# Kernel optimization log

Measured on AMD Instinct MI355X. Metric: run time of the kernel, lower is better.

The kernel has to match this reference:

```python
import jax, jax.numpy as jnp
import numpy as np

CHUNK = 128
KERNEL_EPS = 1e-4
ATTN_EPS = 1e-6


def _gaussian_orthogonal_random_matrix(nb_rows, nb_cols, seed=0):
    # scaling=0: rows of stacked orthogonal blocks, scaled by chi-distributed norms
    rng = np.random.default_rng(seed)
    blocks = []
    n_full = nb_rows // nb_cols
    for _ in range(n_full):
        qm, _ = np.linalg.qr(rng.standard_normal((nb_cols, nb_cols)))
        blocks.append(qm.T)
    rem = nb_rows - n_full * nb_cols
    if rem > 0:
        qm, _ = np.linalg.qr(rng.standard_normal((nb_cols, nb_cols)))
        blocks.append(qm.T[:rem])
    mat = np.concatenate(blocks, axis=0)
    multiplier = np.linalg.norm(rng.standard_normal((nb_rows, nb_cols)), axis=1)
    return (multiplier[:, None] * mat).astype(np.float32)


def softmax_kernel(data, proj, is_query):
    # data: [b,h,n,d], proj: [m,d]
    d = data.shape[-1]
    m = proj.shape[0]
    data_normalizer = d ** -0.25
    ratio = m ** -0.5
    data_dash = jnp.einsum('bhnd,md->bhnm', data * data_normalizer, proj)
    diag_data = (data ** 2).sum(-1, keepdims=True) * 0.5 * (data_normalizer ** 2)
    if is_query:
        stab = jnp.max(data_dash, axis=-1, keepdims=True)
    else:
        stab = jnp.max(data_dash)
    return ratio * (jnp.exp(data_dash - diag_data - stab) + KERNEL_EPS)


def chunked_causal_linear_attention(qf, kf, v):
    # qf,kf: [b,h,n,m]; v: [b,h,n,e]
    b, h, n, m = qf.shape
    e = v.shape[-1]
    nc = n // CHUNK
    to_chunks = lambda t: t.reshape(b, h, nc, CHUNK, -1).transpose(2, 0, 1, 3, 4)
    qc, kc, vc = to_chunks(qf), to_chunks(kf), to_chunks(v)  # [nc,b,h,c,*]

    def step(carry, xs):
        Z, S = carry  # Z: [b,h,m], S: [b,h,m,e]
        q, k, vv = xs
        k_cum = Z[:, :, None, :] + jnp.cumsum(k, axis=2)          # [b,h,c,m]
        D_inv = 1.0 / jnp.einsum('bhcm,bhcm->bhc', q, k_cum + ATTN_EPS)
        ctx = jnp.einsum('bhcm,bhce->bhcme', k, vv)               # [b,h,c,m,e]
        ctx_cum = S[:, :, None, :, :] + jnp.cumsum(ctx, axis=2)
        out = jnp.einsum('bhcme,bhcm,bhc->bhce', ctx_cum, q, D_inv)
        return (k_cum[:, :, -1, :], ctx_cum[:, :, -1, :, :]), out

    Z0 = jnp.zeros((b, h, m), qf.dtype)
    S0 = jnp.zeros((b, h, m, e), qf.dtype)
    (Z, S), outs = jax.lax.scan(jax.checkpoint(step), (Z0, S0), (qc, kc, vc))
    out = outs.transpose(1, 2, 0, 3, 4).reshape(b, h, n, e)
    return out, Z, S


def setup_inputs() -> dict:
    key = jax.random.key(0)
    kq, kk, kv = jax.random.split(key, 3)
    B, H, N, D, M = 2, 8, 4096, 64, 256
    q = jax.random.normal(kq, (B, H, N, D), dtype=jnp.float32)
    k = jax.random.normal(kk, (B, H, N, D), dtype=jnp.float32)
    v = jax.random.normal(kv, (B, H, N, D), dtype=jnp.float32)
    projection_matrix = jnp.asarray(_gaussian_orthogonal_random_matrix(M, D))
    return {"q": q, "k": k, "v": v, "projection_matrix": projection_matrix,
            "inferrring_states": 1}


def reference(q, k, v, projection_matrix, inferrring_states):
    qf = softmax_kernel(q, projection_matrix, is_query=True)
    kf = softmax_kernel(k, projection_matrix, is_query=False)
    out, Z, S = chunked_causal_linear_attention(qf, kf, v)
    return (out, Z, S)
```

## Files before the change

kernel.cpp:

```cpp
#include <hip/hip_runtime.h>

typedef unsigned short ushort_t;
typedef __attribute__((ext_vector_type(8))) short bf16x8;
typedef __attribute__((ext_vector_type(8))) _Float16 f16x8;
typedef __attribute__((ext_vector_type(16))) float f32x16;

#define NORMC 0.35355339059327373f
#define DIAGC 0.0625f
#define RATIO 0.0625f
#define KEPS  1e-4f
#define AEPS  1e-6f
#define KAPPA (RATIO*KEPS)

__device__ __forceinline__ unsigned short f2bf(float f){
  unsigned u = __float_as_uint(f);
  unsigned r = (u + 0x7FFFu + ((u >> 16) & 1u)) >> 16;
  return (unsigned short)r;
}
__device__ __forceinline__ float bf2f(unsigned short h){
  return __uint_as_float(((unsigned)h) << 16);
}
__device__ __forceinline__ unsigned enc_f(float f){
  unsigned u = __float_as_uint(f);
  return (u & 0x80000000u) ? ~u : (u | 0x80000000u);
}
__device__ __forceinline__ float dec_f(unsigned e){
  unsigned b = (e & 0x80000000u) ? (e ^ 0x80000000u) : ~e;
  return __uint_as_float(b);
}
__device__ __forceinline__ unsigned short h2u(_Float16 h){
  union { _Float16 h; unsigned short u; } c; c.h = h; return c.u;
}
__device__ __forceinline__ unsigned pk2h(float a, float b){
  return (unsigned)h2u((_Float16)a) | ((unsigned)h2u((_Float16)b) << 16);
}

__global__ void k_prep(const float* __restrict__ proj, ushort_t* __restrict__ pjh,
                       unsigned* __restrict__ kmax){
  int t = threadIdx.x;
  if (t == 0) *kmax = 0u;
  for (int d = 0; d < 64; ++d){
    float val = NORMC * proj[t*64 + d];
    pjh[t*64 + d] = h2u((_Float16)val);
  }
}

__launch_bounds__(512, 4)
__global__ void k_featQ(const float* __restrict__ q, const ushort_t* __restrict__ pjh,
                        ushort_t* __restrict__ qf)
{
  extern __shared__ char sm[];
  char* Bp = sm;
  char* Xh = sm + 32768;
  char* Xl = sm + 49152;
  float* dsm = (float*)(sm + 65536);
  float* rmx = (float*)(sm + 66048);

  int tid = threadIdx.x;
  int w   = tid >> 6;
  int wr  = w & 3;
  int wc  = w >> 2;
  int lane= tid & 63;
  int l31 = lane & 31;
  int half= lane >> 5;
  int tile = (int)blockIdx.x;
  int row0 = tile * 128;

  for (int i = tid; i < 2048; i += 512){
    int m = i >> 3, c8 = i & 7;
    int rgn = ((m>>5)*4 + (c8>>1))*2 + (c8&1);
    int slot = (m & 31) ^ ((rgn & 7) << 2);
    *(uint4*)(Bp + rgn*512 + slot*16) = *(const uint4*)(pjh + m*64 + c8*8);
  }
  #pragma unroll
  for (int it = 0; it < 4; ++it){
    int g = it*512 + tid;
    int row = g >> 4, c4 = g & 15;
    float4 xv = *(const float4*)(q + (size_t)(row0+row)*64 + c4*4);
    _Float16 h0=(_Float16)xv.x, h1=(_Float16)xv.y, h2=(_Float16)xv.z, h3=(_Float16)xv.w;
    float l0 = xv.x-(float)h0, l1 = xv.y-(float)h1, l2 = xv.z-(float)h2, l3 = xv.w-(float)h3;
    int rgn = ((row>>5)*4 + (c4>>2))*2 + ((c4>>1)&1);
    int off = rgn*512 + (((row&31) ^ ((c4>>1)<<2)))*16 + (c4&1)*8;
    uint2 ph; ph.x = (unsigned)h2u(h0)|((unsigned)h2u(h1)<<16);
              ph.y = (unsigned)h2u(h2)|((unsigned)h2u(h3)<<16);
    uint2 pl; pl.x = pk2h(l0,l1); pl.y = pk2h(l2,l3);
    *(uint2*)(Xh + off) = ph;
    *(uint2*)(Xl + off) = pl;
    float ssq = xv.x*xv.x + xv.y*xv.y + xv.z*xv.z + xv.w*xv.w;
    ssq += __shfl_xor(ssq, 1); ssq += __shfl_xor(ssq, 2);
    ssq += __shfl_xor(ssq, 4); ssq += __shfl_xor(ssq, 8);
    if ((tid & 15) == 0) dsm[row] = ssq;
  }
  __syncthreads();

  f16x8 ah[4], al[4];
  #pragma unroll
  for (int ks = 0; ks < 4; ++ks){
    int rgn = (wr*4+ks)*2+half;
    int off = rgn*512 + ((l31 ^ ((2*ks+half)<<2)))*16;
    ah[ks] = *(const f16x8*)(Xh + off);
    al[ks] = *(const f16x8*)(Xl + off);
  }
  f32x16 acc[4];
  #pragma unroll
  for (int ct=0; ct<4; ++ct){
    #pragma unroll
    for (int r=0; r<16; ++r) acc[ct][r] = 0.f;
  }
  #pragma unroll
  for (int ks = 0; ks < 4; ++ks){
    #pragma unroll
    for (int ct=0; ct<4; ++ct){
      int ctg = wc*4 + ct;
      int rgn = (ctg*4+ks)*2+half;
      f16x8 bv = *(const f16x8*)(Bp + rgn*512 + ((l31 ^ ((2*ks+half)<<2)))*16);
      acc[ct] = __builtin_amdgcn_mfma_f32_32x32x16_f16(ah[ks], bv, acc[ct], 0, 0, 0);
      acc[ct] = __builtin_amdgcn_mfma_f32_32x32x16_f16(al[ks], bv, acc[ct], 0, 0, 0);
    }
  }
  {
    float rmax[16];
    #pragma unroll
    for (int r=0; r<16; ++r){
      float mx = acc[0][r];
      #pragma unroll
      for (int ct=1; ct<4; ++ct) mx = fmaxf(mx, acc[ct][r]);
      #pragma unroll
      for (int s=1; s<32; s<<=1) mx = fmaxf(mx, __shfl_xor(mx, s));
      rmax[r] = mx;
    }
    if (l31 == 0){
      #pragma unroll
      for (int r=0; r<16; ++r)
        rmx[wc*128 + 32*wr + (r&3) + 8*(r>>2) + 4*half] = rmax[r];
    }
  }
  __syncthreads();

  float dgv[16], stv[16];
  #pragma unroll
  for (int r=0; r<16; ++r){
    int lrow = 32*wr + (r&3) + 8*(r>>2) + 4*half;
    dgv[r] = DIAGC * dsm[lrow];
    stv[r] = fmaxf(rmx[lrow], rmx[128+lrow]);
  }

  char* ob = sm;
  #pragma unroll
  for (int r=0; r<16; ++r){
    int lrow = 32*wr + (r&3) + 8*(r>>2) + 4*half;
    #pragma unroll
    for (int ct=0; ct<4; ++ct){
      int col = wc*128 + ct*32 + l31;
      float e = __expf(acc[ct][r] - dgv[r] - stv[r]);
      *(ushort_t*)(ob + lrow*512 + ((col*2) ^ ((lrow&15)<<4))) = f2bf(RATIO*(e + KEPS));
    }
  }
  __syncthreads();
  ushort_t* dst = qf + (size_t)row0*256;
  for (int i = tid; i < 4096; i += 512){
    int row = i >> 5, s = i & 31;
    uint4 d = *(const uint4*)(ob + row*512 + ((s*16) ^ ((row&15)<<4)));
    *(uint4*)(dst + (size_t)row*256 + ((s ^ (row&15)))*8) = d;
  }
}

__launch_bounds__(512, 2)
__global__ void k_chunkF(const float* __restrict__ kk, const float* __restrict__ v,
                         const ushort_t* __restrict__ pjh,
                         ushort_t* __restrict__ kfp, float* __restrict__ Zl,
                         float* __restrict__ Sl, float* __restrict__ vsb,
                         unsigned* __restrict__ kmax, float* __restrict__ lmArr)
{
  extern __shared__ char sm[];
  char* Bp = sm;
  char* Xh = sm + 32768;
  char* Xl = sm + 49152;
  char* ob = sm;
  char* kT = sm + 65536;
  char* vT = sm + 131072;
  float* dsm  = (float*)(sm + 147456);
  float* wred = (float*)(sm + 147968);

  int tid = threadIdx.x;
  int w   = tid >> 6;
  int wr  = w & 3;
  int wc  = w >> 2;
  int lane= tid & 63;
  int l31 = lane & 31;
  int half= lane >> 5;
  int cb  = (int)blockIdx.x;
  int bh  = cb >> 5, j = cb & 31;
  int row0 = bh*4096 + j*128;

  for (int i = tid; i < 2048; i += 512){
    int m = i >> 3, c8 = i & 7;
    int rgn = ((m>>5)*4 + (c8>>1))*2 + (c8&1);
    int slot = (m & 31) ^ ((rgn & 7) << 2);
    *(uint4*)(Bp + rgn*512 + slot*16) = *(const uint4*)(pjh + m*64 + c8*8);
  }
  #pragma unroll
  for (int it = 0; it < 4; ++it){
    int g = it*512 + tid;
    int row = g >> 4, c4 = g & 15;
    float4 xv = *(const float4*)(kk + (size_t)(row0+row)*64 + c4*4);
    _Float16 h0=(_Float16)xv.x, h1=(_Float16)xv.y, h2=(_Float16)xv.z, h3=(_Float16)xv.w;
    float l0 = xv.x-(float)h0, l1 = xv.y-(float)h1, l2 = xv.z-(float)h2, l3 = xv.w-(float)h3;
    int rgn = ((row>>5)*4 + (c4>>2))*2 + ((c4>>1)&1);
    int off = rgn*512 + (((row&31) ^ ((c4>>1)<<2)))*16 + (c4&1)*8;
    uint2 ph; ph.x = (unsigned)h2u(h0)|((unsigned)h2u(h1)<<16);
              ph.y = (unsigned)h2u(h2)|((unsigned)h2u(h3)<<16);
    uint2 pl; pl.x = pk2h(l0,l1); pl.y = pk2h(l2,l3);
    *(uint2*)(Xh + off) = ph;
    *(uint2*)(Xl + off) = pl;
    float ssq = xv.x*xv.x + xv.y*xv.y + xv.z*xv.z + xv.w*xv.w;
    ssq += __shfl_xor(ssq, 1); ssq += __shfl_xor(ssq, 2);
    ssq += __shfl_xor(ssq, 4); ssq += __shfl_xor(ssq, 8);
    if ((tid & 15) == 0) dsm[row] = ssq;
  }
  {
    int e = tid & 63, c0 = tid >> 6;
    int swz = (e & 15) << 4;
    #pragma unroll
    for (int u=0; u<16; ++u){
      int c = c0 + u*8;
      *(ushort_t*)(vT + e*256 + ((c*2) ^ swz)) = f2bf(v[(size_t)(row0+c)*64 + e]);
    }
  }
  __syncthreads();

  f16x8 ah[4], al[4];
  #pragma unroll
  for (int ks = 0; ks < 4; ++ks){
    int rgn = (wr*4+ks)*2+half;
    int off = rgn*512 + ((l31 ^ ((2*ks+half)<<2)))*16;
    ah[ks] = *(const f16x8*)(Xh + off);
    al[ks] = *(const f16x8*)(Xl + off);
  }
  f32x16 acc[4];
  #pragma unroll
  for (int ct=0; ct<4; ++ct){
    #pragma unroll
    for (int r=0; r<16; ++r) acc[ct][r] = 0.f;
  }
  #pragma unroll
  for (int ks = 0; ks < 4; ++ks){
    #pragma unroll
    for (int ct=0; ct<4; ++ct){
      int ctg = wc*4 + ct;
      int rgn = (ctg*4+ks)*2+half;
      f16x8 bv = *(const f16x8*)(Bp + rgn*512 + ((l31 ^ ((2*ks+half)<<2)))*16);
      acc[ct] = __builtin_amdgcn_mfma_f32_32x32x16_f16(ah[ks], bv, acc[ct], 0, 0, 0);
      acc[ct] = __builtin_amdgcn_mfma_f32_32x32x16_f16(al[ks], bv, acc[ct], 0, 0, 0);
    }
  }
  {
    float wm = acc[0][0];
    #pragma unroll
    for (int ct=0; ct<4; ++ct){
      #pragma unroll
      for (int r=0; r<16; ++r) wm = fmaxf(wm, acc[ct][r]);
    }
    #pragma unroll
    for (int s=1; s<32; s<<=1) wm = fmaxf(wm, __shfl_xor(wm, s));
    wm = fmaxf(wm, __shfl_xor(wm, 32));
    if (lane == 0) wred[w] = wm;
  }
  __syncthreads();
  float lmb = wred[0];
  #pragma unroll
  for (int i=1;i<8;++i) lmb = fmaxf(lmb, wred[i]);
  if (tid == 0){
    lmArr[cb] = lmb;
    atomicMax(kmax, enc_f(lmb));
  }
  float dgv[16];
  #pragma unroll
  for (int r=0; r<16; ++r)
    dgv[r] = DIAGC * dsm[32*wr + (r&3) + 8*(r>>2) + 4*half];

  #pragma unroll
  for (int ct=0; ct<4; ++ct){
    int m = wc*128 + ct*32 + l31;
    int swm = (m & 15) << 4;
    #pragma unroll
    for (int g=0; g<4; ++g){
      unsigned pk0=0, pk1=0;
      #pragma unroll
      for (int rr=0; rr<4; ++rr){
        int r = g*4 + rr;
        int c = 32*wr + rr + 8*g + 4*half;
        float e = __expf(acc[ct][r] - dgv[r] - lmb);
        unsigned b = f2bf(e);
        if (rr < 2) pk0 |= b << (16*rr); else pk1 |= b << (16*(rr-2));
        *(ushort_t*)(ob + c*512 + ((m*2) ^ ((c&15)<<4))) = (ushort_t)b;
      }
      int c0 = 32*wr + 8*g + 4*half;
      *(uint2*)(kT + m*256 + ((c0*2) ^ swm)) = make_uint2(pk0, pk1);
    }
  }
  __syncthreads();

  f32x16 accS[2], accz, avs[2];
  #pragma unroll
  for (int et=0;et<2;++et){
    #pragma unroll
    for (int r=0;r<16;++r){ accS[et][r]=0.f; avs[et][r]=0.f; }
  }
  #pragma unroll
  for (int r=0;r<16;++r) accz[r]=0.f;
  bf16x8 onesB, onesA;
  #pragma unroll
  for (int i=0;i<8;++i){
    onesB[i] = (l31==0) ? (short)0x3F80 : (short)0;
    onesA[i] = (short)0x3F80;
  }
  int erow = (w&1)*32 + l31;
  int mc0  = ((w>>1)*2 + 0)*32 + l31;
  int mc1  = ((w>>1)*2 + 1)*32 + l31;
  int mrow = 32*w + l31;
  #pragma unroll
  for (int ks=0; ks<8; ++ks){
    int koff = ks*32 + half*16;
    bf16x8 afv = *(const bf16x8*)(vT + erow*256 + (koff ^ ((erow&15)<<4)));
    bf16x8 bk0 = *(const bf16x8*)(kT + mc0*256 + (koff ^ ((mc0&15)<<4)));
    bf16x8 bk1 = *(const bf16x8*)(kT + mc1*256 + (koff ^ ((mc1&15)<<4)));
    bf16x8 afk = *(const bf16x8*)(kT + mrow*256 + (koff ^ ((mrow&15)<<4)));
    accS[0] = __builtin_amdgcn_mfma_f32_32x32x16_bf16(afv, bk0, accS[0], 0, 0, 0);
    accS[1] = __builtin_amdgcn_mfma_f32_32x32x16_bf16(afv, bk1, accS[1], 0, 0, 0);
    accz    = __builtin_amdgcn_mfma_f32_32x32x16_bf16(afk, onesB, accz, 0, 0, 0);
    if (w == 0){
      bf16x8 bv1 = *(const bf16x8*)(vT + (32+l31)*256 + (koff ^ (((32+l31)&15)<<4)));
      avs[0] = __builtin_amdgcn_mfma_f32_32x32x16_bf16(onesA, afv, avs[0], 0, 0, 0);
      avs[1] = __builtin_amdgcn_mfma_f32_32x32x16_bf16(onesA, bv1, avs[1], 0, 0, 0);
    }
  }
  #pragma unroll
  for (int r=0; r<16; ++r){
    int e = (w&1)*32 + (r&3) + 8*(r>>2) + 4*half;
    Sl[(size_t)cb*16384 + (size_t)e*256 + ((w>>1)*2+0)*32 + l31] = accS[0][r];
    Sl[(size_t)cb*16384 + (size_t)e*256 + ((w>>1)*2+1)*32 + l31] = accS[1][r];
  }
  if (l31 == 0){
    #pragma unroll
    for (int r=0; r<16; ++r){
      int m = 32*w + (r&3) + 8*(r>>2) + 4*half;
      Zl[(size_t)cb*256 + m] = accz[r];
    }
  }
  if (w == 0 && half == 0){
    vsb[(size_t)cb*64 + l31]      = avs[0][0];
    vsb[(size_t)cb*64 + 32 + l31] = avs[1][0];
  }
  {
    ushort_t* dst = kfp + (size_t)row0*256;
    for (int i = tid; i < 4096; i += 512){
      int row = i >> 5, s = i & 31;
      uint4 d = *(const uint4*)(ob + row*512 + ((s*16) ^ ((row&15)<<4)));
      *(uint4*)(dst + (size_t)row*256 + ((s ^ (row&15)))*8) = d;
    }
  }
}

__launch_bounds__(256)
__global__ void k_scan(float* __restrict__ Zl, const float* __restrict__ Sl,
                       const float* __restrict__ vsb, const float* __restrict__ lmArr,
                       const unsigned* __restrict__ kmax,
                       ushort_t* __restrict__ S0b,
                       float* __restrict__ outZ, float* __restrict__ outSt){
  float gm = dec_f(*kmax);
  int t = threadIdx.x;
  int bh = blockIdx.x / 65;
  int s  = blockIdx.x % 65;
  if (s == 64){
    size_t base = (size_t)(bh*32)*256 + t;
    float rz = 0.f;
    #pragma unroll
    for (int j0=0;j0<32;j0+=8){
      float x[8];
      #pragma unroll
      for (int u=0;u<8;++u){
        int cbx = bh*32 + j0 + u;
        float a = RATIO * __expf(lmArr[cbx] - gm);
        x[u] = fmaf(a, Zl[base + (size_t)(j0+u)*256], KAPPA*128.f);
      }
      #pragma unroll
      for (int u=0;u<8;++u){ Zl[base + (size_t)(j0+u)*256] = rz; rz += x[u]; }
    }
    outZ[(size_t)bh*256 + t] = rz;
  } else {
    size_t base = (size_t)(bh*32)*16384 + (size_t)s*256 + t;
    float rs = 0.f;
    #pragma unroll
    for (int j0=0;j0<32;j0+=8){
      float x[8];
      #pragma unroll
      for (int u=0;u<8;++u){
        int cbx = bh*32 + j0 + u;
        float a = RATIO * __expf(lmArr[cbx] - gm);
        x[u] = fmaf(a, Sl[base + (size_t)(j0+u)*16384], KAPPA * vsb[(size_t)cbx*64 + s]);
      }
      #pragma unroll
      for (int u=0;u<8;++u){
        S0b[(size_t)(bh*32 + j0+u)*16384 + (size_t)s*256 + t] = f2bf(rs);
        rs += x[u];
      }
    }
    outSt[(size_t)bh*16384 + (size_t)s*256 + t] = rs;
  }
}

__launch_bounds__(256)
__global__ void k_tr(const float* __restrict__ outSt, float* __restrict__ outS){
  __shared__ float tl[64][65];
  int tid = threadIdx.x;
  int bh = blockIdx.x >> 2, mt = blockIdx.x & 3;
  int m0 = mt*64;
  for (int i = tid; i < 4096; i += 256){
    int e = i >> 6, m = i & 63;
    tl[e][m] = outSt[(size_t)bh*16384 + (size_t)e*256 + m0 + m];
  }
  __syncthreads();
  for (int i = tid; i < 4096; i += 256){
    int m = i >> 6, e = i & 63;
    outS[(size_t)bh*16384 + (size_t)(m0+m)*64 + e] = tl[e][m];
  }
}

__launch_bounds__(512, 2)
__global__ void k_out(const ushort_t* __restrict__ qf, const ushort_t* __restrict__ kfp,
                      const float* __restrict__ v, const ushort_t* __restrict__ S0b,
                      const float* __restrict__ Zp, const float* __restrict__ lmArr,
                      const unsigned* __restrict__ kmax, float* __restrict__ outO)
{
  extern __shared__ char sm[];
  char* Ab   = sm;
  char* qft  = sm + 32768;
  char* vTb  = sm + 32768;
  char* ktb  = sm + 49152;
  char* s0t  = sm + 65536;
  float* rsc = (float*)(sm + 73728);
  ushort_t* z0b = (ushort_t*)(sm + 74752);

  int tid = threadIdx.x;
  int w   = tid >> 6;
  int wr  = w & 3;
  int wc  = w >> 2;
  int lane= tid & 63;
  int l31 = lane & 31;
  int half= lane >> 5;
  int pb  = (int)blockIdx.x;
  int bh  = pb >> 5, j = pb & 31;
  int row0 = bh*4096 + j*128;
  size_t qbase = (size_t)row0*256;

  float gmv = dec_f(*kmax);
  float alpha = RATIO * __expf(lmArr[pb] - gmv);

  if (tid < 256) z0b[tid] = f2bf(Zp[(size_t)pb*256 + tid] + AEPS);

  int ve = tid & 63, vc0 = tid >> 6;
  float vld[16];
  #pragma unroll
  for (int u=0; u<16; ++u)
    vld[u] = v[(size_t)(row0 + vc0 + u*8)*64 + ve];

  int rr0 = (tid*2)   >> 3, c80 = (tid*2)   & 7;
  int rr1 = (tid*2+1) >> 3, c81 = (tid*2+1) & 7;
  int se  = tid >> 3,  sc8 = tid & 7;
  int dsw0 = (c80*16) ^ ((rr0&7)<<4);
  int dsw1 = (c81*16) ^ ((rr1&7)<<4);
  int dsws = (sc8*16) ^ ((se&7)<<4);

  uint4 pq0, pq1, pk0v, pk1v, ps0v;
  #define LOADT(m0_) do { \
    pq0  = *(const uint4*)(qf  + qbase + (size_t)rr0*256 + (m0_) + c80*8); \
    pq1  = *(const uint4*)(qf  + qbase + (size_t)rr1*256 + (m0_) + c81*8); \
    pk0v = *(const uint4*)(kfp + qbase + (size_t)rr0*256 + (m0_) + c80*8); \
    pk1v = *(const uint4*)(kfp + qbase + (size_t)rr1*256 + (m0_) + c81*8); \
    ps0v = *(const uint4*)(S0b + (size_t)pb*16384 + (size_t)se*256 + (m0_) + sc8*8); \
  } while(0)

  f32x16 accA[2], acc2, accQ;
  #pragma unroll
  for (int ct2=0;ct2<2;++ct2){
    #pragma unroll
    for (int r=0;r<16;++r) accA[ct2][r] = 0.f;
  }
  #pragma unroll
  for (int r=0;r<16;++r){ acc2[r] = 0.f; accQ[r] = 0.f; }

  int arow = 32*wr + l31;
  LOADT(0);

  #pragma unroll
  for (int mt=0; mt<4; ++mt){
    int m0 = mt*64;
    __syncthreads();
    *(uint4*)(qft + rr0*128 + dsw0) = pq0;
    *(uint4*)(qft + rr1*128 + dsw1) = pq1;
    *(uint4*)(ktb + rr0*128 + dsw0) = pk0v;
    *(uint4*)(ktb + rr1*128 + dsw1) = pk1v;
    *(uint4*)(s0t + se*128  + dsws) = ps0v;
    __syncthreads();
    if (mt < 3) LOADT((mt+1)*64);
    #pragma unroll
    for (int ks=0;ks<4;++ks){
      int ko = ks*32 + half*16;
      bf16x8 af = *(const bf16x8*)(qft + arow*128 + (ko ^ ((arow&7)<<4)));
      {
        int er = wc*32 + l31;
        bf16x8 bS = *(const bf16x8*)(s0t + er*128 + (ko ^ ((er&7)<<4)));
        acc2 = __builtin_amdgcn_mfma_f32_32x32x16_bf16(af, bS, acc2, 0, 0, 0);
      }
      {
        bf16x8 zb = {};
        if (l31 == 0) zb = *(const bf16x8*)((const char*)z0b + m0*2 + ko);
        if (l31 == 1){
          #pragma unroll
          for (int i2=0;i2<8;++i2) zb[i2] = (short)0x3F80;
        }
        accQ = __builtin_amdgcn_mfma_f32_32x32x16_bf16(af, zb, accQ, 0, 0, 0);
      }
      #pragma unroll
      for (int ct2=0;ct2<2;++ct2){
        int c = wc*2 + ct2;
        if (c <= wr){
          int br = c*32 + l31;
          bf16x8 bk = *(const bf16x8*)(ktb + br*128 + (ko ^ ((br&7)<<4)));
          accA[ct2] = __builtin_amdgcn_mfma_f32_32x32x16_bf16(af, bk, accA[ct2], 0, 0, 0);
        }
      }
    }
  }
  #undef LOADT

  float qzv[16], qfsv[16];
  #pragma unroll
  for (int r=0;r<16;++r){
    qzv[r]  = __shfl(accQ[r], half*32 + 0);
    qfsv[r] = __shfl(accQ[r], half*32 + 1);
  }

  {
    float p[16];
    #pragma unroll
    for (int r=0;r<16;++r) p[r]=0.f;
    #pragma unroll
    for (int ct2=0;ct2<2;++ct2){
      int c = wc*2 + ct2;
      if (c <= wr){
        #pragma unroll
        for (int r=0;r<16;++r){
          int grow = 32*wr + (r&3) + 8*(r>>2) + 4*half;
          int col  = c*32 + l31;
          float mval = (col <= grow) ? fmaf(alpha, accA[ct2][r], KAPPA*qfsv[r]) : 0.f;
          p[r] += mval;
          *(ushort_t*)(Ab + grow*256 + ((col*2) ^ ((grow&15)<<4))) = f2bf(mval);
        }
      }
    }
    #pragma unroll
    for (int s2=1;s2<32;s2<<=1){
      #pragma unroll
      for (int r=0;r<16;++r) p[r] += __shfl_xor(p[r], s2);
    }
    if (l31 == 0){
      #pragma unroll
      for (int r=0;r<16;++r)
        rsc[wc*128 + 32*wr + (r&3) + 8*(r>>2) + 4*half] = p[r];
    }
  }
  __syncthreads();

  {
    int swz = (ve & 15) << 4;
    #pragma unroll
    for (int u=0; u<16; ++u){
      int c = vc0 + u*8;
      *(ushort_t*)(vTb + ve*256 + ((c*2) ^ swz)) = f2bf(vld[u]);
    }
  }
  __syncthreads();

  #pragma unroll
  for (int ks=0; ks<8; ++ks){
    if (ks <= 2*wr + 1){
      bf16x8 af = *(const bf16x8*)(Ab + arow*256 + ((ks*32 + half*16) ^ ((arow&15)<<4)));
      int er = wc*32 + l31;
      bf16x8 bv = *(const bf16x8*)(vTb + er*256 + ((ks*32 + half*16) ^ ((er&15)<<4)));
      acc2 = __builtin_amdgcn_mfma_f32_32x32x16_bf16(af, bv, acc2, 0, 0, 0);
    }
  }

  #pragma unroll
  for (int r=0;r<16;++r){
    int grow = 32*wr + (r&3) + 8*(r>>2) + 4*half;
    float dv = 1.0f / (rsc[grow] + rsc[128+grow] + qzv[r]);
    outO[(size_t)(row0+grow)*64 + wc*32 + l31] = acc2[r] * dv;
  }
}

extern "C" void kernel_launch(void* const* d_in, const int* in_sizes, int n_in,
                              void* d_out, int out_size, void* d_ws, size_t ws_size,
                              hipStream_t stream){
  (void)in_sizes; (void)n_in; (void)out_size; (void)ws_size;
  const float* q    = (const float*)d_in[0];
  const float* k    = (const float*)d_in[1];
  const float* v    = (const float*)d_in[2];
  const float* proj = (const float*)d_in[3];

  char* ws = (char*)d_ws;
  unsigned* kmax = (unsigned*)ws;
  float*    lmA  = (float*)(ws + 256);
  ushort_t* pjh  = (ushort_t*)(ws + 4096);
  ushort_t* kfp  = (ushort_t*)(ws + 65792);
  float*    Zl   = (float*)(ws + 33620224);
  float*    Sl   = (float*)(ws + 34144512);
  ushort_t* S0b  = (ushort_t*)(ws + 67698944);
  float*    vsb  = (float*)(ws + 84476160);
  float*    oSt  = (float*)(ws + 84607232);
  ushort_t* qfb  = (ushort_t*)(ws + 88801536);

  float* outO = (float*)d_out;
  float* outZ = outO + (size_t)2*8*4096*64;
  float* outS = outZ + 2*8*256;

  hipFuncSetAttribute((const void*)k_featQ,  hipFuncAttributeMaxDynamicSharedMemorySize, 67072);
  hipFuncSetAttribute((const void*)k_chunkF, hipFuncAttributeMaxDynamicSharedMemorySize, 148480);
  hipFuncSetAttribute((const void*)k_out,    hipFuncAttributeMaxDynamicSharedMemorySize, 75264);

  k_prep  <<<1,     256, 0, stream>>>(proj, pjh, kmax);
  k_featQ <<<512,   512, 67072, stream>>>(q, pjh, qfb);
  k_chunkF<<<512,   512, 148480, stream>>>(k, v, pjh, kfp, Zl, Sl, vsb, kmax, lmA);
  k_scan  <<<16*65, 256, 0, stream>>>(Zl, Sl, vsb, lmA, kmax, S0b, outZ, oSt);
  k_tr    <<<64,    256, 0, stream>>>(oSt, outS);
  k_out   <<<512,   512, 75264, stream>>>(qfb, kfp, v, S0b, Zl, lmA, kmax, outO);
}
```

Baseline: 106.8 us.

## Split k_out Q·S0 and Q·K passes to cut register pressure

The single fused loop over the feature dimension, which held accA[2], acc2 and accQ live together, is split into two passes: first Q·S0 and Q·Z, then Q·K^T. The per-row normaliser values go through shared memory instead of registers. V is now loaded just before its transpose rather than held in 16 registers across the whole kernel. The launch-bounds hint asks for 4 blocks per SM instead of 2. The aim is higher occupancy, at the cost of reloading the Q tiles a second time, extra barriers, and a slightly larger shared-memory footprint that may itself cap residency.

```diff
diff --git a/kernel.cpp b/kernel.cpp
--- a/kernel.cpp
+++ b/kernel.cpp
@@ -427,7 +427,7 @@
   }
 }
 
-__launch_bounds__(512, 2)
+__launch_bounds__(512, 4)
 __global__ void k_out(const ushort_t* __restrict__ qf, const ushort_t* __restrict__ kfp,
                       const float* __restrict__ v, const ushort_t* __restrict__ S0b,
                       const float* __restrict__ Zp, const float* __restrict__ lmArr,
@@ -441,6 +441,8 @@
   char* s0t  = sm + 65536;
   float* rsc = (float*)(sm + 73728);
   ushort_t* z0b = (ushort_t*)(sm + 74752);
+  float* qzl = (float*)(sm + 75264);
+  float* qfl = (float*)(sm + 75776);
 
   int tid = threadIdx.x;
   int w   = tid >> 6;
@@ -459,102 +461,126 @@
 
   if (tid < 256) z0b[tid] = f2bf(Zp[(size_t)pb*256 + tid] + AEPS);
 
-  int ve = tid & 63, vc0 = tid >> 6;
-  float vld[16];
-  #pragma unroll
-  for (int u=0; u<16; ++u)
-    vld[u] = v[(size_t)(row0 + vc0 + u*8)*64 + ve];
-
   int rr0 = (tid*2)   >> 3, c80 = (tid*2)   & 7;
   int rr1 = (tid*2+1) >> 3, c81 = (tid*2+1) & 7;
   int se  = tid >> 3,  sc8 = tid & 7;
   int dsw0 = (c80*16) ^ ((rr0&7)<<4);
   int dsw1 = (c81*16) ^ ((rr1&7)<<4);
   int dsws = (sc8*16) ^ ((se&7)<<4);
-
-  uint4 pq0, pq1, pk0v, pk1v, ps0v;
-  #define LOADT(m0_) do { \
-    pq0  = *(const uint4*)(qf  + qbase + (size_t)rr0*256 + (m0_) + c80*8); \
-    pq1  = *(const uint4*)(qf  + qbase + (size_t)rr1*256 + (m0_) + c81*8); \
-    pk0v = *(const uint4*)(kfp + qbase + (size_t)rr0*256 + (m0_) + c80*8); \
-    pk1v = *(const uint4*)(kfp + qbase + (size_t)rr1*256 + (m0_) + c81*8); \
-    ps0v = *(const uint4*)(S0b + (size_t)pb*16384 + (size_t)se*256 + (m0_) + sc8*8); \
-  } while(0)
-
-  f32x16 accA[2], acc2, accQ;
+  int arow = 32*wr + l31;
+
+  f32x16 acc2, accQ;
+  #pragma unroll
+  for (int r=0;r<16;++r){ acc2[r] = 0.f; accQ[r] = 0.f; }
+  {
+    uint4 pq0, pq1, ps0;
+    pq0 = *(const uint4*)(qf  + qbase + (size_t)rr0*256 + c80*8);
+    pq1 = *(const uint4*)(qf  + qbase + (size_t)rr1*256 + c81*8);
+    ps0 = *(const uint4*)(S0b + (size_t)pb*16384 + (size_t)se*256 + sc8*8);
+    #pragma unroll
+    for (int mt=0; mt<4; ++mt){
+      int m0 = mt*64;
+      __syncthreads();
+      *(uint4*)(qft + rr0*128 + dsw0) = pq0;
+      *(uint4*)(qft + rr1*128 + dsw1) = pq1;
+      *(uint4*)(s0t + se*128  + dsws) = ps0;
+      __syncthreads();
+      if (mt < 3){
+        int mn = (mt+1)*64;
+        pq0 = *(const uint4*)(qf  + qbase + (size_t)rr0*256 + mn + c80*8);
+        pq1 = *(const uint4*)(qf  + qbase + (size_t)rr1*256 + mn + c81*8);
+        ps0 = *(const uint4*)(S0b + (size_t)pb*16384 + (size_t)se*256 + mn + sc8*8);
+      }
+      #pragma unroll
+      for (int ks=0;ks<4;++ks){
+        int ko = ks*32 + half*16;
+        bf16x8 af = *(const bf16x8*)(qft + arow*128 + (ko ^ ((arow&7)<<4)));
+        {
+          int er = wc*32 + l31;
+          bf16x8 bS = *(const bf16x8*)(s0t + er*128 + (ko ^ ((er&7)<<4)));
+          acc2 = __builtin_amdgcn_mfma_f32_32x32x16_bf16(af, bS, acc2, 0, 0, 0);
+        }
+        {
+          bf16x8 zb = {};
+          if (l31 == 0) zb = *(const bf16x8*)((const char*)z0b + m0*2 + ko);
+          if (l31 == 1){
+            #pragma unroll
+            for (int i2=0;i2<8;++i2) zb[i2] = (short)0x3F80;
+          }
+          accQ = __builtin_amdgcn_mfma_f32_32x32x16_bf16(af, zb, accQ, 0, 0, 0);
+        }
+      }
+    }
+  }
+  #pragma unroll
+  for (int r=0;r<16;++r){
+    float qz  = __shfl(accQ[r], half*32 + 0);
+    float qfs = __shfl(accQ[r], half*32 + 1);
+    if (wc == 0 && l31 == 0){
+      int grow = 32*wr + (r&3) + 8*(r>>2) + 4*half;
+      qzl[grow] = qz;
+      qfl[grow] = qfs;
+    }
+  }
+
+  f32x16 accA[2];
   #pragma unroll
   for (int ct2=0;ct2<2;++ct2){
     #pragma unroll
     for (int r=0;r<16;++r) accA[ct2][r] = 0.f;
   }
-  #pragma unroll
-  for (int r=0;r<16;++r){ acc2[r] = 0.f; accQ[r] = 0.f; }
-
-  int arow = 32*wr + l31;
-  LOADT(0);
-
-  #pragma unroll
-  for (int mt=0; mt<4; ++mt){
-    int m0 = mt*64;
-    __syncthreads();
-    *(uint4*)(qft + rr0*128 + dsw0) = pq0;
-    *(uint4*)(qft + rr1*128 + dsw1) = pq1;
-    *(uint4*)(ktb + rr0*128 + dsw0) = pk0v;
-    *(uint4*)(ktb + rr1*128 + dsw1) = pk1v;
-    *(uint4*)(s0t + se*128  + dsws) = ps0v;
-    __syncthreads();
-    if (mt < 3) LOADT((mt+1)*64);
-    #pragma unroll
-    for (int ks=0;ks<4;++ks){
-      int ko = ks*32 + half*16;
-      bf16x8 af = *(const bf16x8*)(qft + arow*128 + (ko ^ ((arow&7)<<4)));
-      {
-        int er = wc*32 + l31;
-        bf16x8 bS = *(const bf16x8*)(s0t + er*128 + (ko ^ ((er&7)<<4)));
-        acc2 = __builtin_amdgcn_mfma_f32_32x32x16_bf16(af, bS, acc2, 0, 0, 0);
-      }
-      {
-        bf16x8 zb = {};
-        if (l31 == 0) zb = *(const bf16x8*)((const char*)z0b + m0*2 + ko);
-        if (l31 == 1){
-          #pragma unroll
-          for (int i2=0;i2<8;++i2) zb[i2] = (short)0x3F80;
+  {
+    uint4 pq0, pq1, pk0v, pk1v;
+    pq0  = *(const uint4*)(qf  + qbase + (size_t)rr0*256 + c80*8);
+    pq1  = *(const uint4*)(qf  + qbase + (size_t)rr1*256 + c81*8);
+    pk0v = *(const uint4*)(kfp + qbase + (size_t)rr0*256 + c80*8);
+    pk1v = *(const uint4*)(kfp + qbase + (size_t)rr1*256 + c81*8);
+    #pragma unroll
+    for (int mt=0; mt<4; ++mt){
+      __syncthreads();
+      *(uint4*)(qft + rr0*128 + dsw0) = pq0;
+      *(uint4*)(qft + rr1*128 + dsw1) = pq1;
+      *(uint4*)(ktb + rr0*128 + dsw0) = pk0v;
+      *(uint4*)(ktb + rr1*128 + dsw1) = pk1v;
+      __syncthreads();
+      if (mt < 3){
+        int mn = (mt+1)*64;
+        pq0  = *(const uint4*)(qf  + qbase + (size_t)rr0*256 + mn + c80*8);
+        pq1  = *(const uint4*)(qf  + qbase + (size_t)rr1*256 + mn + c81*8);
+        pk0v = *(const uint4*)(kfp + qbase + (size_t)rr0*256 + mn + c80*8);
+        pk1v = *(const uint4*)(kfp + qbase + (size_t)rr1*256 + mn + c81*8);
+      }
+      #pragma unroll
+      for (int ks=0;ks<4;++ks){
+        int ko = ks*32 + half*16;
+        bf16x8 af = *(const bf16x8*)(qft + arow*128 + (ko ^ ((arow&7)<<4)));
+        #pragma unroll
+        for (int ct2=0;ct2<2;++ct2){
+          int c = wc*2 + ct2;
+          if (c <= wr){
+            int br = c*32 + l31;
+            bf16x8 bk = *(const bf16x8*)(ktb + br*128 + (ko ^ ((br&7)<<4)));
+            accA[ct2] = __builtin_amdgcn_mfma_f32_32x32x16_bf16(af, bk, accA[ct2], 0, 0, 0);
+          }
         }
-        accQ = __builtin_amdgcn_mfma_f32_32x32x16_bf16(af, zb, accQ, 0, 0, 0);
-      }
+      }
+    }
+  }
+
+  {
+    float p[16];
+    #pragma unroll
+    for (int r=0;r<16;++r) p[r]=0.f;
+    #pragma unroll
+    for (int r=0;r<16;++r){
+      int grow = 32*wr + (r&3) + 8*(r>>2) + 4*half;
+      float qfs = qfl[grow];
       #pragma unroll
       for (int ct2=0;ct2<2;++ct2){
         int c = wc*2 + ct2;
         if (c <= wr){
-          int br = c*32 + l31;
-          bf16x8 bk = *(const bf16x8*)(ktb + br*128 + (ko ^ ((br&7)<<4)));
-          accA[ct2] = __builtin_amdgcn_mfma_f32_32x32x16_bf16(af, bk, accA[ct2], 0, 0, 0);
-        }
-      }
-    }
-  }
-  #undef LOADT
-
-  float qzv[16], qfsv[16];
-  #pragma unroll
-  for (int r=0;r<16;++r){
-    qzv[r]  = __shfl(accQ[r], half*32 + 0);
-    qfsv[r] = __shfl(accQ[r], half*32 + 1);
-  }
-
-  {
-    float p[16];
-    #pragma unroll
-    for (int r=0;r<16;++r) p[r]=0.f;
-    #pragma unroll
-    for (int ct2=0;ct2<2;++ct2){
-      int c = wc*2 + ct2;
-      if (c <= wr){
-        #pragma unroll
-        for (int r=0;r<16;++r){
-          int grow = 32*wr + (r&3) + 8*(r>>2) + 4*half;
-          int col  = c*32 + l31;
-          float mval = (col <= grow) ? fmaf(alpha, accA[ct2][r], KAPPA*qfsv[r]) : 0.f;
+          int col = c*32 + l31;
+          float mval = (col <= grow) ? fmaf(alpha, accA[ct2][r], KAPPA*qfs) : 0.f;
           p[r] += mval;
           *(ushort_t*)(Ab + grow*256 + ((col*2) ^ ((grow&15)<<4))) = f2bf(mval);
         }
@@ -574,11 +600,13 @@
   __syncthreads();
 
   {
+    int ve = tid & 63, vc0 = tid >> 6;
     int swz = (ve & 15) << 4;
     #pragma unroll
     for (int u=0; u<16; ++u){
       int c = vc0 + u*8;
-      *(ushort_t*)(vTb + ve*256 + ((c*2) ^ swz)) = f2bf(vld[u]);
+      float vv = v[(size_t)(row0 + c)*64 + ve];
+      *(ushort_t*)(vTb + ve*256 + ((c*2) ^ swz)) = f2bf(vv);
     }
   }
   __syncthreads();
@@ -596,7 +624,7 @@
   #pragma unroll
   for (int r=0;r<16;++r){
     int grow = 32*wr + (r&3) + 8*(r>>2) + 4*half;
-    float dv = 1.0f / (rsc[grow] + rsc[128+grow] + qzv[r]);
+    float dv = 1.0f / (rsc[grow] + rsc[128+grow] + qzl[grow]);
     outO[(size_t)(row0+grow)*64 + wc*32 + l31] = acc2[r] * dv;
   }
 }
@@ -628,12 +656,12 @@
 
   hipFuncSetAttribute((const void*)k_featQ,  hipFuncAttributeMaxDynamicSharedMemorySize, 67072);
   hipFuncSetAttribute((const void*)k_chunkF, hipFuncAttributeMaxDynamicSharedMemorySize, 148480);
-  hipFuncSetAttribute((const void*)k_out,    hipFuncAttributeMaxDynamicSharedMemorySize, 75264);
+  hipFuncSetAttribute((const void*)k_out,    hipFuncAttributeMaxDynamicSharedMemorySize, 76288);
 
   k_prep  <<<1,     256, 0, stream>>>(proj, pjh, kmax);
   k_featQ <<<512,   512, 67072, stream>>>(q, pjh, qfb);
   k_chunkF<<<512,   512, 148480, stream>>>(k, v, pjh, kfp, Zl, Sl, vsb, kmax, lmA);
   k_scan  <<<16*65, 256, 0, stream>>>(Zl, Sl, vsb, lmA, kmax, S0b, outZ, oSt);
   k_tr    <<<64,    256, 0, stream>>>(oSt, outS);
-  k_out   <<<512,   512, 75264, stream>>>(qfb, kfp, v, S0b, Zl, lmA, kmax, outO);
-}
+  k_out   <<<512,   512, 76288, stream>>>(qfb, kfp, v, S0b, Zl, lmA, kmax, outO);
+}
```

After: 192.5 us. +80.3%, slower.
